# Performance work log

Measured on AMD Instinct MI355X. Metric: run time of the kernel, lower is better.

## Reference

```python
import jax, jax.numpy as jnp
import numpy as np

B, C_IN, H, W = 8, 64, 64, 64
C_OUT = 128
K, STRIDE, PAD = 3, 1, 1
GRID_MIN, GRID_MAX, NUM_GRIDS = -2.0, 2.0, 8
FEAT = C_IN * K * K  # 576


def setup_inputs() -> dict:
    key = jax.random.key(0)
    k1, k2, k3 = jax.random.split(key, 3)
    x = jax.random.normal(k1, (B, C_IN, H, W), dtype=jnp.float32)
    grid = jnp.linspace(GRID_MIN, GRID_MAX, NUM_GRIDS, dtype=jnp.float32)
    spline_weight = jax.random.normal(k2, (FEAT * NUM_GRIDS, C_OUT), dtype=jnp.float32) * 0.1
    # nn.Linear default init ~ U(-1/sqrt(in), 1/sqrt(in)); stored as (in, out) for x @ W
    bound = 1.0 / np.sqrt(FEAT)
    kw, kb = jax.random.split(k3)
    base_w = jax.random.uniform(kw, (FEAT, C_OUT), dtype=jnp.float32, minval=-bound, maxval=bound)
    base_b = jax.random.uniform(kb, (C_OUT,), dtype=jnp.float32, minval=-bound, maxval=bound)
    return {"x": x, "grid": grid, "spline_weight": spline_weight,
            "base_w": base_w, "base_b": base_b}


def reference(x, grid, spline_weight, base_w, base_b):
    b, c, h, w = x.shape
    # F.unfold equivalent: patches in (channel, kh, kw) channel-major order.
    patches = jax.lax.conv_general_dilated_patches(
        x, filter_shape=(K, K), window_strides=(STRIDE, STRIDE),
        padding=((PAD, PAD), (PAD, PAD)))  # [B, C*K*K, H', W']
    oh, ow = patches.shape[2], patches.shape[3]
    # -> [B*L, FEAT] rows, matching unfold().transpose(1,2).reshape(...)
    p = patches.reshape(b, FEAT, oh * ow).transpose(0, 2, 1).reshape(-1, FEAT)
    # RBF basis expansion: exp(-((x - g) / h)^2), h = grid spacing
    denom = (GRID_MAX - GRID_MIN) / (NUM_GRIDS - 1)
    basis = jnp.exp(-(((p[:, :, None] - grid) / denom) ** 2))  # [N, FEAT, G]
    ret = basis.reshape(p.shape[0], FEAT * NUM_GRIDS) @ spline_weight  # [N, C_OUT]
    ret = ret + jax.nn.silu(p) @ base_w + base_b
    # [B, L, C_OUT] -> [B, C_OUT, H', W']
    out = ret.reshape(b, oh * ow, C_OUT).transpose(0, 2, 1).reshape(b, C_OUT, oh, ow)
    return out
```

## Files before the change

kernel.cpp:

```cpp
#include <hip/hip_runtime.h>

#define C_IN   64
#define HW_DIM 64
#define C_OUT  128
#define NG     8
#define BM     64
#define NSPL_STEPS 72
#define NSTEPS 81
#define NBASE  9
#define NPAD   66

#define XE_XP   64
#define XE_GRP  4224
#define XE_YP   33792
#define XE_B    2230272
#define SE_XP   64
#define SE_YP   4224
#define SE_B    278784

#define WT_BYTES 1327104
#define XE_OFF   WT_BYTES
#define XE_BYTES (XE_B * 8 * 2)
#define SE_OFF   (XE_OFF + XE_BYTES)

typedef __attribute__((ext_vector_type(8))) __bf16 bf16x8;
typedef __attribute__((ext_vector_type(4))) float  f32x4;

__global__ __launch_bounds__(256)
void prep_wt(const float* __restrict__ sw, const float* __restrict__ bw,
             __bf16* __restrict__ wt3)
{
  const int bid  = blockIdx.x;
  const int t    = threadIdx.x;
  const int wc   = t >> 6;
  const int lane = t & 63;
  const int l15  = lane & 15;
  const int g4   = lane >> 4;
#pragma unroll
  for (int n = 0; n < 2; ++n)
#pragma unroll
    for (int ks = 0; ks < 2; ++ks) {
      const int co = wc * 32 + n * 16 + l15;
      const int q  = ks * 4 + g4;
      bf16x8 v;
      if (bid < NSPL_STEPS) {
        const int grp = bid / 9, j = bid - 9 * grp;
        const int c   = grp * 8 + q;
#pragma unroll
        for (int e = 0; e < 8; ++e)
          v[e] = (__bf16)sw[(size_t)((c * 9 + j) * 8 + e) * C_OUT + co];
      } else {
        const int j = bid - NSPL_STEPS;
#pragma unroll
        for (int e = 0; e < 8; ++e)
          v[e] = (__bf16)bw[(size_t)((q * 8 + e) * 9 + j) * C_OUT + co];
      }
      *(bf16x8*)(wt3 + (size_t)bid * 8192 + wc * 2048 + (n * 2 + ks) * 512
                 + lane * 8) = v;
    }
}

__global__ __launch_bounds__(256)
void expand_xe(const float* __restrict__ x, const float* __restrict__ grid,
               __bf16* __restrict__ xe)
{
  __shared__ __align__(16) __bf16 buf[528 * 8];
  const int bid = blockIdx.x;
  const int b   = bid / 528;
  const int r   = bid - b * 528;
  const int yp  = r >> 3;
  const int grp = r & 7;
  const int t   = threadIdx.x;

  float gv[NG];
#pragma unroll
  for (int g = 0; g < NG; ++g) gv[g] = grid[g];

  for (int i = t; i < 528; i += 256) {
    const int xp = i >> 3;
    const int cg = i & 7;
    const int c  = grp * 8 + cg;
    float p = 0.f;
    if (xp >= 1 && xp <= HW_DIM && yp >= 1 && yp <= HW_DIM)
      p = x[(size_t)(b * C_IN + c) * (HW_DIM * HW_DIM)
            + (yp - 1) * HW_DIM + (xp - 1)];
    bf16x8 v;
#pragma unroll
    for (int g = 0; g < NG; ++g) {
      const float z = 1.75f * (p - gv[g]);
      v[g] = (__bf16)__expf(-z * z);
    }
    *(bf16x8*)(buf + i * 8) = v;
  }
  __syncthreads();
  __bf16* dst = xe + (size_t)b * XE_B + yp * XE_YP + grp * XE_GRP;
  for (int i = t; i < 528; i += 256)
    *(bf16x8*)(dst + i * 8) = *(const bf16x8*)(buf + i * 8);
}

__global__ __launch_bounds__(256)
void expand_se(const float* __restrict__ x, __bf16* __restrict__ se)
{
  __shared__ __align__(16) __bf16 buf[4224];
  const int bid = blockIdx.x;
  const int b   = bid / 66;
  const int yp  = bid - b * 66;
  const int t   = threadIdx.x;

  for (int i = t; i < 4224; i += 256) {
    const int xp = i >> 6;
    const int c  = i & 63;
    float p = 0.f;
    if (xp >= 1 && xp <= HW_DIM && yp >= 1 && yp <= HW_DIM)
      p = x[(size_t)(b * C_IN + c) * (HW_DIM * HW_DIM)
            + (yp - 1) * HW_DIM + (xp - 1)];
    const float e = __expf(-p);
    buf[i] = (__bf16)(p * __builtin_amdgcn_rcpf(1.f + e));
  }
  __syncthreads();
  __bf16* dst = se + (size_t)b * SE_B + yp * SE_YP;
  for (int i = t; i < 528; i += 256)
    *(bf16x8*)(dst + i * 8) = *(const bf16x8*)(buf + i * 8);
}

static __device__ __forceinline__ void gload16(const __bf16* g, __bf16* l) {
  __builtin_amdgcn_global_load_lds(
      (const __attribute__((address_space(1))) void*)g,
      (__attribute__((address_space(3))) void*)l, 16, 0, 0);
}

#define WAITBAR6() do {                                      \
    asm volatile("s_waitcnt vmcnt(6)" ::: "memory");         \
    __builtin_amdgcn_s_barrier();                            \
    __builtin_amdgcn_sched_barrier(0);                       \
  } while (0)

__global__ __launch_bounds__(256, 2)
void kan_gemm(const __bf16* __restrict__ xe, const __bf16* __restrict__ se,
              const __bf16* __restrict__ wt3, const float* __restrict__ base_b,
              float* __restrict__ out)
{
  __shared__ __align__(16) __bf16 As[3][BM][64];

  const int t    = threadIdx.x;
  const int lane = t & 63;
  const int wid  = t >> 6;
  const int l15  = lane & 15;
  const int g4   = lane >> 4;

  const int bid = blockIdx.x;
  const int swz = (bid & 7) * 64 + (bid >> 3);
  const int b   = swz >> 6;
  const int y0  = swz & 63;

  const int px0 = t >> 3;
  const int qs  = (t & 7) ^ (px0 & 7);

  f32x4 acc[2][4];
#pragma unroll
  for (int n = 0; n < 2; ++n)
#pragma unroll
    for (int m = 0; m < 4; ++m)
      acc[n][m] = f32x4{0.f, 0.f, 0.f, 0.f};

  const __bf16* xeb = xe + (size_t)b * XE_B + y0 * XE_YP;

  auto stageA = [&](int buf, int s) {
    const int grp = s / 9, j = s - 9 * grp;
    const int kh = j / 3, kw = j - 3 * (j / 3);
    const __bf16* src = xeb + kh * XE_YP + grp * XE_GRP + kw * XE_XP
                      + px0 * 64 + qs * 8;
    __bf16* dst = &As[buf][0][0] + t * 8;
    gload16(src,        dst);
    gload16(src + 2048, dst + 2048);
  };

  auto loadB = [&](bf16x8 (&wf)[2][2], int step) {
    const __bf16* wb = wt3 + (size_t)step * 8192 + wid * 2048 + lane * 8;
#pragma unroll
    for (int n = 0; n < 2; ++n)
#pragma unroll
      for (int ks = 0; ks < 2; ++ks)
        wf[n][ks] = *(const bf16x8*)(wb + (n * 2 + ks) * 512);
  };

  auto compute = [&](int buf, bf16x8 (&wf)[2][2]) {
    bf16x8 xf[4][2];
#pragma unroll
    for (int ks = 0; ks < 2; ++ks)
#pragma unroll
      for (int m = 0; m < 4; ++m) {
        const int pr = m * 16 + l15;
        xf[m][ks] = *(const bf16x8*)(&As[buf][pr][(((ks * 4 + g4) ^ (pr & 7)) * 8)]);
      }
#pragma unroll
    for (int ks = 0; ks < 2; ++ks)
#pragma unroll
      for (int n = 0; n < 2; ++n)
#pragma unroll
        for (int m = 0; m < 4; ++m)
          acc[n][m] = __builtin_amdgcn_mfma_f32_16x16x32_bf16(
              wf[n][ks], xf[m][ks], acc[n][m], 0, 0, 0);
  };

  bf16x8 wA[2][2], wB[2][2], wC[2][2];
  stageA(0, 0); loadB(wA, 0);
  stageA(1, 1); loadB(wB, 1);
  WAITBAR6();

  for (int s = 0; s < NSPL_STEPS - 3; s += 3) {
    stageA(2, s + 2); loadB(wC, s + 2);
    compute(0, wA);
    WAITBAR6();
    stageA(0, s + 3); loadB(wA, s + 3);
    compute(1, wB);
    WAITBAR6();
    stageA(1, s + 4); loadB(wB, s + 4);
    compute(2, wC);
    WAITBAR6();
  }
  stageA(2, 71); loadB(wC, 71);
  compute(0, wA);
  WAITBAR6();
  compute(1, wB);
  asm volatile("s_waitcnt vmcnt(0)" ::: "memory");
  __builtin_amdgcn_s_barrier();
  __builtin_amdgcn_sched_barrier(0);
  compute(2, wC);

  const __bf16* seb = se + (size_t)b * SE_B + y0 * SE_YP;
  auto stageBase = [&](int buf, int j) {
    const int kh = j / 3, kw = j - 3 * (j / 3);
    const int px = t & 63;
    const __bf16* src = seb + kh * SE_YP + (px + kw) * SE_XP;
#pragma unroll
    for (int h = 0; h < 2; ++h) {
      const int q = (t >> 6) + h * 4;
      const bf16x8 v = *(const bf16x8*)(src + q * 8);
      *(bf16x8*)(&As[buf][px][((q ^ (px & 7)) * 8)]) = v;
    }
  };

  stageBase(0, 0);
  __syncthreads();
  for (int bs = 0; bs < NBASE; ++bs) {
    const int cb = bs & 1;
    if (bs + 1 < NBASE) stageBase(cb ^ 1, bs + 1);
    loadB(wA, NSPL_STEPS + bs);
    compute(cb, wA);
    __syncthreads();
  }

#pragma unroll
  for (int n = 0; n < 2; ++n) {
    const int co = wid * 32 + n * 16 + g4 * 4;
#pragma unroll
    for (int m = 0; m < 4; ++m) {
      const int pl = m * 16 + l15;
      float* o = out + (size_t)(b * C_OUT + co) * 4096 + y0 * 64 + pl;
#pragma unroll
      for (int i = 0; i < 4; ++i)
        o[(size_t)i * 4096] = acc[n][m][i] + base_b[co + i];
    }
  }
}

extern "C" void kernel_launch(void* const* d_in, const int* in_sizes, int n_in,
                              void* d_out, int out_size, void* d_ws, size_t ws_size,
                              hipStream_t stream) {
  const float* x    = (const float*)d_in[0];
  const float* grid = (const float*)d_in[1];
  const float* sw   = (const float*)d_in[2];
  const float* bw   = (const float*)d_in[3];
  const float* bb   = (const float*)d_in[4];
  float* out = (float*)d_out;

  __bf16* wt3 = (__bf16*)d_ws;
  __bf16* xe  = (__bf16*)((char*)d_ws + XE_OFF);
  __bf16* se  = (__bf16*)((char*)d_ws + SE_OFF);

  prep_wt<<<NSTEPS, 256, 0, stream>>>(sw, bw, wt3);
  expand_xe<<<4224, 256, 0, stream>>>(x, grid, xe);
  expand_se<<<528, 256, 0, stream>>>(x, se);
  kan_gemm<<<512, 256, 0, stream>>>(xe, se, wt3, bb, out);
}
```

Before: 82.40 us.

## Split spline reduction across two blocks per 2-row tile with atomic accumulation

```diff
diff --git a/kernel.cpp b/kernel.cpp
--- a/kernel.cpp
+++ b/kernel.cpp
@@ -4,9 +4,10 @@
 #define HW_DIM 64
 #define C_OUT  128
 #define NG     8
-#define BM     64
+#define BM     128
 #define NSPL_STEPS 72
 #define NSTEPS 81
+#define NHALF  36
 #define NBASE  9
 #define NPAD   66
 
@@ -32,7 +33,7 @@
 {
   const int bid  = blockIdx.x;
   const int t    = threadIdx.x;
-  const int wc   = t >> 6;
+  const int nq   = t >> 6;
   const int lane = t & 63;
   const int l15  = lane & 15;
   const int g4   = lane >> 4;
@@ -40,7 +41,7 @@
   for (int n = 0; n < 2; ++n)
 #pragma unroll
     for (int ks = 0; ks < 2; ++ks) {
-      const int co = wc * 32 + n * 16 + l15;
+      const int co = nq * 32 + n * 16 + l15;
       const int q  = ks * 4 + g4;
       bf16x8 v;
       if (bid < NSPL_STEPS) {
@@ -55,7 +56,7 @@
         for (int e = 0; e < 8; ++e)
           v[e] = (__bf16)bw[(size_t)((q * 8 + e) * 9 + j) * C_OUT + co];
       }
-      *(bf16x8*)(wt3 + (size_t)bid * 8192 + wc * 2048 + (n * 2 + ks) * 512
+      *(bf16x8*)(wt3 + (size_t)bid * 8192 + nq * 2048 + (n * 2 + ks) * 512
                  + lane * 8) = v;
     }
 }
@@ -123,6 +124,15 @@
     *(bf16x8*)(dst + i * 8) = *(const bf16x8*)(buf + i * 8);
 }
 
+__global__ __launch_bounds__(256)
+void init_out(const float* __restrict__ bb, float* __restrict__ out)
+{
+  const int i4 = blockIdx.x * 256 + threadIdx.x;
+  const int e  = i4 * 4;
+  const float v = bb[(e >> 12) & 127];
+  *(f32x4*)(out + e) = f32x4{v, v, v, v};
+}
+
 static __device__ __forceinline__ void gload16(const __bf16* g, __bf16* l) {
   __builtin_amdgcn_global_load_lds(
       (const __attribute__((address_space(1))) void*)g,
@@ -135,10 +145,9 @@
     __builtin_amdgcn_sched_barrier(0);                       \
   } while (0)
 
-__global__ __launch_bounds__(256, 2)
+__global__ __launch_bounds__(512, 4)
 void kan_gemm(const __bf16* __restrict__ xe, const __bf16* __restrict__ se,
-              const __bf16* __restrict__ wt3, const float* __restrict__ base_b,
-              float* __restrict__ out)
+              const __bf16* __restrict__ wt3, float* __restrict__ out)
 {
   __shared__ __align__(16) __bf16 As[3][BM][64];
 
@@ -147,11 +156,16 @@
   const int wid  = t >> 6;
   const int l15  = lane & 15;
   const int g4   = lane >> 4;
+  const int mh   = wid >> 2;
+  const int nq   = wid & 3;
 
   const int bid = blockIdx.x;
   const int swz = (bid & 7) * 64 + (bid >> 3);
-  const int b   = swz >> 6;
-  const int y0  = swz & 63;
+  const int kh  = swz & 1;
+  const int rb  = swz >> 1;
+  const int b   = rb >> 5;
+  const int y0  = (rb & 31) * 2;
+  const int S0  = kh * NHALF;
 
   const int px0 = t >> 3;
   const int qs  = (t & 7) ^ (px0 & 7);
@@ -167,16 +181,16 @@
 
   auto stageA = [&](int buf, int s) {
     const int grp = s / 9, j = s - 9 * grp;
-    const int kh = j / 3, kw = j - 3 * (j / 3);
-    const __bf16* src = xeb + kh * XE_YP + grp * XE_GRP + kw * XE_XP
+    const int kt = j / 3, kw = j - 3 * kt;
+    const __bf16* src = xeb + kt * XE_YP + grp * XE_GRP + kw * XE_XP
                       + px0 * 64 + qs * 8;
     __bf16* dst = &As[buf][0][0] + t * 8;
-    gload16(src,        dst);
-    gload16(src + 2048, dst + 2048);
+    gload16(src,         dst);
+    gload16(src + XE_YP, dst + 4096);
   };
 
   auto loadB = [&](bf16x8 (&wf)[2][2], int step) {
-    const __bf16* wb = wt3 + (size_t)step * 8192 + wid * 2048 + lane * 8;
+    const __bf16* wb = wt3 + (size_t)step * 8192 + nq * 2048 + lane * 8;
 #pragma unroll
     for (int n = 0; n < 2; ++n)
 #pragma unroll
@@ -190,7 +204,7 @@
     for (int ks = 0; ks < 2; ++ks)
 #pragma unroll
       for (int m = 0; m < 4; ++m) {
-        const int pr = m * 16 + l15;
+        const int pr = mh * 64 + m * 16 + l15;
         xf[m][ks] = *(const bf16x8*)(&As[buf][pr][(((ks * 4 + g4) ^ (pr & 7)) * 8)]);
       }
 #pragma unroll
@@ -204,22 +218,22 @@
   };
 
   bf16x8 wA[2][2], wB[2][2], wC[2][2];
-  stageA(0, 0); loadB(wA, 0);
-  stageA(1, 1); loadB(wB, 1);
+  stageA(0, S0 + 0); loadB(wA, S0 + 0);
+  stageA(1, S0 + 1); loadB(wB, S0 + 1);
   WAITBAR6();
 
-  for (int s = 0; s < NSPL_STEPS - 3; s += 3) {
-    stageA(2, s + 2); loadB(wC, s + 2);
+  for (int s = 0; s < NHALF - 3; s += 3) {
+    stageA(2, S0 + s + 2); loadB(wC, S0 + s + 2);
     compute(0, wA);
     WAITBAR6();
-    stageA(0, s + 3); loadB(wA, s + 3);
+    stageA(0, S0 + s + 3); loadB(wA, S0 + s + 3);
     compute(1, wB);
     WAITBAR6();
-    stageA(1, s + 4); loadB(wB, s + 4);
+    stageA(1, S0 + s + 4); loadB(wB, S0 + s + 4);
     compute(2, wC);
     WAITBAR6();
   }
-  stageA(2, 71); loadB(wC, 71);
+  stageA(2, S0 + 35); loadB(wC, S0 + 35);
   compute(0, wA);
   WAITBAR6();
   compute(1, wB);
@@ -228,39 +242,45 @@
   __builtin_amdgcn_sched_barrier(0);
   compute(2, wC);
 
-  const __bf16* seb = se + (size_t)b * SE_B + y0 * SE_YP;
-  auto stageBase = [&](int buf, int j) {
-    const int kh = j / 3, kw = j - 3 * (j / 3);
-    const int px = t & 63;
-    const __bf16* src = seb + kh * SE_YP + (px + kw) * SE_XP;
-#pragma unroll
-    for (int h = 0; h < 2; ++h) {
-      const int q = (t >> 6) + h * 4;
-      const bf16x8 v = *(const bf16x8*)(src + q * 8);
-      *(bf16x8*)(&As[buf][px][((q ^ (px & 7)) * 8)]) = v;
+  if (kh == 1) {
+    const __bf16* seb = se + (size_t)b * SE_B + y0 * SE_YP;
+    auto stageBase = [&](int buf, int j) {
+      const int kt = j / 3, kw = j - 3 * kt;
+      const int px = t & 127;
+      const __bf16* src = seb + (kt + (px >> 6)) * SE_YP
+                        + ((px & 63) + kw) * SE_XP;
+#pragma unroll
+      for (int h = 0; h < 2; ++h) {
+        const int gslot = (t >> 7) * 2 + h;
+        const int q     = gslot ^ (px & 7);
+        const bf16x8 v  = *(const bf16x8*)(src + q * 8);
+        *(bf16x8*)(&As[buf][px][gslot * 8]) = v;
+      }
+    };
+
+    stageBase(0, 0);
+    __syncthreads();
+    bf16x8 wD[2][2];
+    for (int bs = 0; bs < NBASE; ++bs) {
+      const int cb = bs & 1;
+      if (bs + 1 < NBASE) stageBase(cb ^ 1, bs + 1);
+      loadB(wD, NSPL_STEPS + bs);
+      compute(cb, wD);
+      __syncthreads();
     }
-  };
-
-  stageBase(0, 0);
-  __syncthreads();
-  for (int bs = 0; bs < NBASE; ++bs) {
-    const int cb = bs & 1;
-    if (bs + 1 < NBASE) stageBase(cb ^ 1, bs + 1);
-    loadB(wA, NSPL_STEPS + bs);
-    compute(cb, wA);
-    __syncthreads();
   }
 
 #pragma unroll
   for (int n = 0; n < 2; ++n) {
-    const int co = wid * 32 + n * 16 + g4 * 4;
+    const int co = nq * 32 + n * 16 + g4 * 4;
 #pragma unroll
     for (int m = 0; m < 4; ++m) {
-      const int pl = m * 16 + l15;
-      float* o = out + (size_t)(b * C_OUT + co) * 4096 + y0 * 64 + pl;
+      const int y = y0 + mh;
+      const int xcoord = m * 16 + l15;
+      float* o = out + (size_t)(b * C_OUT + co) * 4096 + y * 64 + xcoord;
 #pragma unroll
       for (int i = 0; i < 4; ++i)
-        o[(size_t)i * 4096] = acc[n][m][i] + base_b[co + i];
+        unsafeAtomicAdd(o + (size_t)i * 4096, acc[n][m][i]);
     }
   }
 }
@@ -282,5 +302,6 @@
   prep_wt<<<NSTEPS, 256, 0, stream>>>(sw, bw, wt3);
   expand_xe<<<4224, 256, 0, stream>>>(x, grid, xe);
   expand_se<<<528, 256, 0, stream>>>(x, se);
-  kan_gemm<<<512, 256, 0, stream>>>(xe, se, wt3, bb, out);
-}
+  init_out<<<4096, 256, 0, stream>>>(bb, out);
+  kan_gemm<<<512, 512, 0, stream>>>(xe, se, wt3, out);
+}
```

New measurement: 102.0 us. +23.8%, slower.
